# Kernel optimization log

Hardware: AMD Instinct MI355X
Metric: run time of the kernel (lower is better)

Reference implementation:

```python
import jax, jax.numpy as jnp
import numpy as np
import math

NUM_HEADS = 16
LOGIT_SCALE_MAX = math.log(1.0 / 0.01)  # log(100)
EPS = 1e-12


def _l2norm(x):
    # F.normalize(x, dim=-1): x / max(||x||_2, eps)
    n = jnp.sqrt(jnp.sum(x * x, axis=-1, keepdims=True))
    return x / jnp.maximum(n, EPS)


def setup_inputs() -> dict:
    key = jax.random.key(0)
    ks = jax.random.split(key, 6)
    N, B, C = 1024, 4, 1024
    scale = (C // NUM_HEADS) ** -0.5
    return {
        "query": jax.random.normal(ks[0], (N, B, C), jnp.float32),
        "key": jax.random.normal(ks[1], (N, B, C), jnp.float32),
        "value": jax.random.normal(ks[2], (N, B, C), jnp.float32),
        "in_proj_w": jax.random.normal(ks[3], (3 * C, C), jnp.float32) * scale,
        "in_proj_b": jnp.zeros((3 * C,), jnp.float32),
        "logit_scale": jnp.log(10.0) * jnp.ones((NUM_HEADS, 1, 1), jnp.float32),
        "out_w": jax.random.normal(ks[4], (C, C), jnp.float32) * scale,
        "out_b": jnp.zeros((C,), jnp.float32),
    }


def reference(query, key, value, in_proj_w, in_proj_b, logit_scale, out_w, out_b):
    N, B, C = query.shape
    H = NUM_HEADS
    hd = C // H
    # packed in-projection, split into q/k/v pieces
    w_q, w_k, w_v = jnp.split(in_proj_w, 3, axis=0)
    b_q, b_k, b_v = jnp.split(in_proj_b, 3, axis=0)
    q = query @ w_q.T + b_q          # (N, B, C)
    k = key @ w_k.T + b_k
    v = value @ w_v.T + b_v
    # (N, B, C) -> (B*H, N, hd)
    q = q.reshape(N, B * H, hd).swapaxes(0, 1)
    k = k.reshape(N, B * H, hd).swapaxes(0, 1)
    v = v.reshape(N, B * H, hd).swapaxes(0, 1)
    # cosine-similarity scores with learnable per-head logit scale
    attn = jnp.einsum('bqd,bkd->bqk', _l2norm(q), _l2norm(k))  # (B*H, N, N)
    ls = jnp.exp(jnp.minimum(logit_scale, LOGIT_SCALE_MAX))     # (H,1,1)
    attn = (attn.reshape(B, H, N, N) * ls).reshape(B * H, N, N)
    attn = jax.nn.softmax(attn, axis=-1)
    x = jnp.einsum('bqk,bkd->bqd', attn, v)                     # (B*H, N, hd)
    x = x.swapaxes(0, 1).reshape(N, B, C)
    return x @ out_w.T + out_b
```

## Files before the change

kernel.cpp:

```cpp
#include <hip/hip_runtime.h>


typedef _Float16 f16x8 __attribute__((ext_vector_type(8)));
typedef float    f32x4 __attribute__((ext_vector_type(4)));

#define LOG2E 1.4426950408889634f
#define LOGMAX 4.6051702f

#define GLOAD16(g, l) \
    __builtin_amdgcn_global_load_lds((__attribute__((address_space(1))) void*)(g), \
                                     (__attribute__((address_space(3))) void*)(l), 16, 0, 0)

__device__ __forceinline__ unsigned short f2h(float x) {
    union { _Float16 h; unsigned short u; } cv;
    cv.h = (_Float16)x;
    return cv.u;
}

__global__ __launch_bounds__(256) void cvt_all(
    const float* __restrict__ q, const float* __restrict__ k,
    const float* __restrict__ v, const float* __restrict__ w,
    const float* __restrict__ ow,
    unsigned short* __restrict__ qbf, unsigned short* __restrict__ kbf,
    unsigned short* __restrict__ vbf, unsigned short* __restrict__ wbf,
    unsigned short* __restrict__ owbf)
{
    int b = blockIdx.x;
    const float* src; unsigned short* dst; int idx;
    if      (b < 4096)  { src = q;  dst = qbf;  idx = b; }
    else if (b < 8192)  { src = k;  dst = kbf;  idx = b - 4096; }
    else if (b < 12288) { src = v;  dst = vbf;  idx = b - 8192; }
    else if (b < 15360) { src = w;  dst = wbf;  idx = b - 12288; }
    else                { src = ow; dst = owbf; idx = b - 15360; }
    int i = idx * 256 + threadIdx.x;
    float4 val = ((const float4*)src)[i];
    ushort4 o;
    o.x = f2h(val.x); o.y = f2h(val.y); o.z = f2h(val.z); o.w = f2h(val.w);
    ((ushort4*)dst)[i] = o;
}

__global__ __launch_bounds__(256) void proj_gemm(
    const unsigned short* __restrict__ qbf, const unsigned short* __restrict__ kbf,
    const unsigned short* __restrict__ vbf, const unsigned short* __restrict__ wbf,
    const float* __restrict__ bias, const float* __restrict__ lsc,
    unsigned short* __restrict__ qn, unsigned short* __restrict__ kn,
    unsigned short* __restrict__ vT)
{
    __shared__ __align__(16) unsigned short AsmF[128 * 64];
    __shared__ __align__(16) unsigned short BsmF[128 * 64];
    int tid = threadIdx.x;
    int lane = tid & 63, wave = tid >> 6;
    int lr = lane & 15, lq = lane >> 4;
    int wr = wave >> 1, wc = wave & 1;

    int lin = blockIdx.x;
    int xcd = lin & 7, s = lin >> 3;
    int xt = s & 7, yy = (s >> 3) & 3, z = s >> 5;
    int m0 = (xcd * 4 + yy) * 128, n0 = xt * 128;

    const unsigned short* A = (z == 0) ? qbf : (z == 1) ? kbf : vbf;
    const unsigned short* W = wbf + (size_t)z * 1024 * 1024;

    int rl = lane >> 3;
    int cg = ((lane & 7) ^ rl) << 3;
    const unsigned short* gA = A + (size_t)(m0 + wave * 32 + rl) * 1024 + cg;
    const unsigned short* gB = W + (size_t)(n0 + wave * 32 + rl) * 1024 + cg;
    unsigned short* lA = &AsmF[wave * 32 * 64];
    unsigned short* lB = &BsmF[wave * 32 * 64];

    int swz = lr & 7;
    int c0 = (lq ^ swz) << 3;
    int c1 = ((lq ^ 4) ^ swz) << 3;

    f32x4 acc[4][4];
    for (int i = 0; i < 4; i++) for (int j = 0; j < 4; j++) acc[i][j] = (f32x4){0.f, 0.f, 0.f, 0.f};

    for (int ki = 0; ki < 16; ++ki) {
        for (int j = 0; j < 4; ++j) {
            GLOAD16(gA + ki * 64 + j * 8192, lA + j * 512);
            GLOAD16(gB + ki * 64 + j * 8192, lB + j * 512);
        }
        __syncthreads();
        for (int kc = 0; kc < 2; ++kc) {
            int co = kc ? c1 : c0;
            f16x8 af[4], bfr[4];
            for (int mi = 0; mi < 4; ++mi) af[mi]  = *(const f16x8*)&AsmF[(wr * 64 + mi * 16 + lr) * 64 + co];
            for (int ni = 0; ni < 4; ++ni) bfr[ni] = *(const f16x8*)&BsmF[(wc * 64 + ni * 16 + lr) * 64 + co];
            for (int mi = 0; mi < 4; ++mi)
                for (int ni = 0; ni < 4; ++ni)
                    acc[mi][ni] = __builtin_amdgcn_mfma_f32_16x16x32_f16(af[mi], bfr[ni], acc[mi][ni], 0, 0, 0);
        }
        __syncthreads();
    }

    int h = (n0 >> 6) + wc;
    float bv[4];
    for (int ni = 0; ni < 4; ++ni) bv[ni] = bias[z * 1024 + n0 + wc * 64 + ni * 16 + lr];
    for (int mi = 0; mi < 4; ++mi)
        for (int ni = 0; ni < 4; ++ni)
            for (int r = 0; r < 4; ++r) acc[mi][ni][r] += bv[ni];

    float lsfac = __expf(fminf(lsc[h], LOGMAX)) * LOG2E;

    for (int mi = 0; mi < 4; ++mi)
        for (int r = 0; r < 4; ++r) {
            int row = m0 + wr * 64 + mi * 16 + lq * 4 + r;
            int n = row >> 2, b = row & 3;
            int bh = b * 16 + h;
            if (z < 2) {
                float ss = 0.f;
                for (int ni = 0; ni < 4; ++ni) ss += acc[mi][ni][r] * acc[mi][ni][r];
                for (int off = 1; off < 16; off <<= 1) ss += __shfl_xor(ss, off);
                float scale = 1.0f / fmaxf(sqrtf(ss), 1e-12f);
                if (z == 0) scale *= lsfac;
                unsigned short* dst = (z == 0) ? qn : kn;
                for (int ni = 0; ni < 4; ++ni)
                    dst[(size_t)bh * 65536 + (size_t)n * 64 + ni * 16 + lr] = f2h(acc[mi][ni][r] * scale);
            } else {
                for (int ni = 0; ni < 4; ++ni)
                    vT[(size_t)bh * 65536 + (size_t)(ni * 16 + lr) * 1024 + n] = f2h(acc[mi][ni][r]);
            }
        }
}

__global__ __launch_bounds__(256) void flash_kernel(
    const unsigned short* __restrict__ qn, const unsigned short* __restrict__ kn,
    const unsigned short* __restrict__ vT, const float* __restrict__ lsc,
    unsigned short* __restrict__ xb)
{
    __shared__ __align__(16) unsigned short K_flat[64 * 64];
    __shared__ __align__(16) unsigned short V_flat[64 * 64];
    __shared__ __align__(16) unsigned short P_lds[4][2][16][72];
    int tid = threadIdx.x;
    int lane = tid & 63, wave = tid >> 6;
    int lr = lane & 15, lq = lane >> 4;

    int lin = blockIdx.x;
    int xcd = lin & 7, s = lin >> 3;
    int qt = s & 7, bh = xcd * 8 + (s >> 3);
    int q0 = qt * 128;

    float off = __expf(fminf(lsc[bh & 15], LOGMAX)) * LOG2E - 12.0f;
    f32x4 initv = (f32x4){-off, -off, -off, -off};

    f16x8 qf[2][2];
    for (int g = 0; g < 2; ++g)
        for (int kc = 0; kc < 2; ++kc)
            qf[g][kc] = *(const f16x8*)(qn + (size_t)bh * 65536 +
                          (size_t)(q0 + g * 64 + wave * 16 + lr) * 64 + kc * 32 + lq * 8);

    int rl = lane >> 3;
    int cg = ((lane & 7) ^ rl) << 3;
    const unsigned short* gK = kn + (size_t)bh * 65536 + (size_t)(wave * 16 + rl) * 64 + cg;
    const unsigned short* gV = vT + (size_t)bh * 65536 + (size_t)(wave * 16 + rl) * 1024 + cg;
    unsigned short* lK = &K_flat[wave * 16 * 64];
    unsigned short* lV = &V_flat[wave * 16 * 64];
    int swz = lr & 7;
    int c0 = (lq ^ swz) << 3;
    int c1 = ((lq ^ 4) ^ swz) << 3;

    f32x4 o[2][4];
    for (int g = 0; g < 2; ++g) for (int i = 0; i < 4; i++) o[g][i] = (f32x4){0.f, 0.f, 0.f, 0.f};
    float lsum[2] = {0.f, 0.f};

    for (int kt = 0; kt < 16; ++kt) {
        for (int j = 0; j < 2; ++j) {
            GLOAD16(gK + kt * 4096 + j * 512,  lK + j * 512);
            GLOAD16(gV + kt * 64  + j * 8192,  lV + j * 512);
        }
        __syncthreads();

        f32x4 sc[2][4];
        for (int ct = 0; ct < 4; ++ct) {
            for (int kc = 0; kc < 2; ++kc) {
                f16x8 kf = *(const f16x8*)&K_flat[(ct * 16 + lr) * 64 + (kc ? c1 : c0)];
                for (int g = 0; g < 2; ++g)
                    sc[g][ct] = __builtin_amdgcn_mfma_f32_16x16x32_f16(
                        kf, qf[g][kc], kc == 0 ? initv : sc[g][ct], 0, 0, 0);
            }
        }

        for (int g = 0; g < 2; ++g)
            for (int ct = 0; ct < 4; ++ct) {
                float p0 = exp2f(sc[g][ct][0]), p1 = exp2f(sc[g][ct][1]);
                float p2 = exp2f(sc[g][ct][2]), p3 = exp2f(sc[g][ct][3]);
                lsum[g] += (p0 + p1) + (p2 + p3);
                ushort4 pw;
                pw.x = f2h(p0); pw.y = f2h(p1); pw.z = f2h(p2); pw.w = f2h(p3);
                *(ushort4*)&P_lds[wave][g][lr][ct * 16 + lq * 4] = pw;
            }

        f16x8 pf[2][2];
        for (int g = 0; g < 2; ++g)
            for (int kc = 0; kc < 2; ++kc)
                pf[g][kc] = *(const f16x8*)&P_lds[wave][g][lr][kc * 32 + lq * 8];
        for (int nt = 0; nt < 4; ++nt)
            for (int kc = 0; kc < 2; ++kc) {
                f16x8 vf = *(const f16x8*)&V_flat[(nt * 16 + lr) * 64 + (kc ? c1 : c0)];
                for (int g = 0; g < 2; ++g)
                    o[g][nt] = __builtin_amdgcn_mfma_f32_16x16x32_f16(vf, pf[g][kc], o[g][nt], 0, 0, 0);
            }
        __syncthreads();
    }

    int b = bh >> 4, h = bh & 15;
    for (int g = 0; g < 2; ++g) {
        float ls = lsum[g];
        ls += __shfl_xor(ls, 16);
        ls += __shfl_xor(ls, 32);
        float inv = 1.0f / ls;
        size_t m = (size_t)(q0 + g * 64 + wave * 16 + lr) * 4 + b;
        for (int nt = 0; nt < 4; ++nt) {
            ushort4 w;
            w.x = f2h(o[g][nt][0] * inv); w.y = f2h(o[g][nt][1] * inv);
            w.z = f2h(o[g][nt][2] * inv); w.w = f2h(o[g][nt][3] * inv);
            *(ushort4*)(xb + m * 1024 + h * 64 + nt * 16 + lq * 4) = w;
        }
    }
}

__global__ __launch_bounds__(256) void out_gemm(
    const unsigned short* __restrict__ xb, const unsigned short* __restrict__ owbf,
    const float* __restrict__ bias, float* __restrict__ outp)
{
    __shared__ __align__(16) unsigned short AsmF[128 * 64];
    __shared__ __align__(16) unsigned short BsmF[64 * 64];
    int tid = threadIdx.x;
    int lane = tid & 63, wave = tid >> 6;
    int lr = lane & 15, lq = lane >> 4;

    int lin = blockIdx.x;
    int xcd = lin & 7, s = lin >> 3;
    int xt = s & 15, yy = s >> 4;
    int m0 = (xcd * 4 + yy) * 128, n0 = xt * 64;

    int rl = lane >> 3;
    int cg = ((lane & 7) ^ rl) << 3;
    const unsigned short* gA = xb   + (size_t)(m0 + wave * 32 + rl) * 1024 + cg;
    const unsigned short* gB = owbf + (size_t)(n0 + wave * 16 + rl) * 1024 + cg;
    unsigned short* lA = &AsmF[wave * 32 * 64];
    unsigned short* lB = &BsmF[wave * 16 * 64];
    int swz = lr & 7;
    int c0 = (lq ^ swz) << 3;
    int c1 = ((lq ^ 4) ^ swz) << 3;

    f32x4 acc[2][4];
    for (int i = 0; i < 2; i++) for (int j = 0; j < 4; j++) acc[i][j] = (f32x4){0.f, 0.f, 0.f, 0.f};

    for (int ki = 0; ki < 16; ++ki) {
        for (int j = 0; j < 4; ++j)
            GLOAD16(gA + ki * 64 + j * 8192, lA + j * 512);
        for (int j = 0; j < 2; ++j)
            GLOAD16(gB + ki * 64 + j * 8192, lB + j * 512);
        __syncthreads();
        for (int kc = 0; kc < 2; ++kc) {
            int co = kc ? c1 : c0;
            f16x8 af[2], bfr[4];
            for (int mi = 0; mi < 2; ++mi) af[mi]  = *(const f16x8*)&AsmF[(wave * 32 + mi * 16 + lr) * 64 + co];
            for (int ni = 0; ni < 4; ++ni) bfr[ni] = *(const f16x8*)&BsmF[(ni * 16 + lr) * 64 + co];
            for (int mi = 0; mi < 2; ++mi)
                for (int ni = 0; ni < 4; ++ni)
                    acc[mi][ni] = __builtin_amdgcn_mfma_f32_16x16x32_f16(af[mi], bfr[ni], acc[mi][ni], 0, 0, 0);
        }
        __syncthreads();
    }
    for (int mi = 0; mi < 2; ++mi)
        for (int ni = 0; ni < 4; ++ni)
            for (int r = 0; r < 4; ++r) {
                int row = m0 + wave * 32 + mi * 16 + lq * 4 + r;
                int col = n0 + ni * 16 + lr;
                outp[(size_t)row * 1024 + col] = acc[mi][ni][r] + bias[col];
            }
}

extern "C" void kernel_launch(void* const* d_in, const int* in_sizes, int n_in,
                              void* d_out, int out_size, void* d_ws, size_t ws_size,
                              hipStream_t stream) {
    const float* query = (const float*)d_in[0];
    const float* key   = (const float*)d_in[1];
    const float* value = (const float*)d_in[2];
    const float* ipw   = (const float*)d_in[3];
    const float* ipb   = (const float*)d_in[4];
    const float* lsc   = (const float*)d_in[5];
    const float* ow    = (const float*)d_in[6];
    const float* ob    = (const float*)d_in[7];
    float* outp = (float*)d_out;

    char* ws = (char*)d_ws;
    unsigned short* qbf  = (unsigned short*)(ws);
    unsigned short* kbf  = (unsigned short*)(ws + 8388608);
    unsigned short* vbf  = (unsigned short*)(ws + 16777216);
    unsigned short* wbf  = (unsigned short*)(ws + 25165824);
    unsigned short* owbf = (unsigned short*)(ws + 31457280);
    unsigned short* qn   = (unsigned short*)(ws + 33554432);
    unsigned short* kn   = (unsigned short*)(ws + 41943040);
    unsigned short* vT   = (unsigned short*)(ws + 50331648);
    unsigned short* xbuf = (unsigned short*)(ws + 58720256);

    cvt_all<<<16384, 256, 0, stream>>>(query, key, value, ipw, ow,
                                       qbf, kbf, vbf, wbf, owbf);
    proj_gemm<<<768, 256, 0, stream>>>(qbf, kbf, vbf, wbf, ipb, lsc, qn, kn, vT);
    flash_kernel<<<512, 256, 0, stream>>>(qn, kn, vT, lsc, xbuf);
    out_gemm<<<512, 256, 0, stream>>>(xbuf, owbf, ob, outp);
}
```

Baseline: 207.0 us.

## Double-buffer K/V tiles in flash kernel and use packed fp16 conversion

Splits the K and V LDS tiles into two buffers so the next tile's global-to-LDS loads are issued while the current tile is computed, with one barrier per iteration instead of two. It also switches to the raw exp2 builtin and packed round-toward-zero fp16 conversion for the probabilities, and raises wave priority around the MFMA blocks. The intent is to hide load latency and cut VALU work in the softmax step. The cost is twice the LDS for K/V, which may lower occupancy, plus RTZ rounding instead of round-to-nearest.

```diff
diff --git a/kernel.cpp b/kernel.cpp
--- a/kernel.cpp
+++ b/kernel.cpp
@@ -2,6 +2,7 @@
 
 
 typedef _Float16 f16x8 __attribute__((ext_vector_type(8)));
+typedef __fp16   h16x2 __attribute__((ext_vector_type(2)));
 typedef float    f32x4 __attribute__((ext_vector_type(4)));
 
 #define LOG2E 1.4426950408889634f
@@ -128,8 +129,8 @@
     const unsigned short* __restrict__ vT, const float* __restrict__ lsc,
     unsigned short* __restrict__ xb)
 {
-    __shared__ __align__(16) unsigned short K_flat[64 * 64];
-    __shared__ __align__(16) unsigned short V_flat[64 * 64];
+    __shared__ __align__(16) unsigned short K_flat[2][64 * 64];
+    __shared__ __align__(16) unsigned short V_flat[2][64 * 64];
     __shared__ __align__(16) unsigned short P_lds[4][2][16][72];
     int tid = threadIdx.x;
     int lane = tid & 63, wave = tid >> 6;
@@ -153,8 +154,6 @@
     int cg = ((lane & 7) ^ rl) << 3;
     const unsigned short* gK = kn + (size_t)bh * 65536 + (size_t)(wave * 16 + rl) * 64 + cg;
     const unsigned short* gV = vT + (size_t)bh * 65536 + (size_t)(wave * 16 + rl) * 1024 + cg;
-    unsigned short* lK = &K_flat[wave * 16 * 64];
-    unsigned short* lV = &V_flat[wave * 16 * 64];
     int swz = lr & 7;
     int c0 = (lq ^ swz) << 3;
     int c1 = ((lq ^ 4) ^ swz) << 3;
@@ -163,44 +162,65 @@
     for (int g = 0; g < 2; ++g) for (int i = 0; i < 4; i++) o[g][i] = (f32x4){0.f, 0.f, 0.f, 0.f};
     float lsum[2] = {0.f, 0.f};
 
+    {
+        unsigned short* lK = &K_flat[0][wave * 16 * 64];
+        unsigned short* lV = &V_flat[0][wave * 16 * 64];
+        for (int j = 0; j < 2; ++j) {
+            GLOAD16(gK + j * 512,  lK + j * 512);
+            GLOAD16(gV + j * 8192, lV + j * 512);
+        }
+    }
+
     for (int kt = 0; kt < 16; ++kt) {
-        for (int j = 0; j < 2; ++j) {
-            GLOAD16(gK + kt * 4096 + j * 512,  lK + j * 512);
-            GLOAD16(gV + kt * 64  + j * 8192,  lV + j * 512);
-        }
-        __syncthreads();
+        int cur = kt & 1;
+        __syncthreads();
+
+        if (kt < 15) {
+            unsigned short* lK = &K_flat[cur ^ 1][wave * 16 * 64];
+            unsigned short* lV = &V_flat[cur ^ 1][wave * 16 * 64];
+            for (int j = 0; j < 2; ++j) {
+                GLOAD16(gK + (kt + 1) * 4096 + j * 512,  lK + j * 512);
+                GLOAD16(gV + (kt + 1) * 64  + j * 8192,  lV + j * 512);
+            }
+        }
 
         f32x4 sc[2][4];
+        __builtin_amdgcn_s_setprio(1);
         for (int ct = 0; ct < 4; ++ct) {
             for (int kc = 0; kc < 2; ++kc) {
-                f16x8 kf = *(const f16x8*)&K_flat[(ct * 16 + lr) * 64 + (kc ? c1 : c0)];
+                f16x8 kf = *(const f16x8*)&K_flat[cur][(ct * 16 + lr) * 64 + (kc ? c1 : c0)];
                 for (int g = 0; g < 2; ++g)
                     sc[g][ct] = __builtin_amdgcn_mfma_f32_16x16x32_f16(
                         kf, qf[g][kc], kc == 0 ? initv : sc[g][ct], 0, 0, 0);
             }
         }
+        __builtin_amdgcn_s_setprio(0);
 
         for (int g = 0; g < 2; ++g)
             for (int ct = 0; ct < 4; ++ct) {
-                float p0 = exp2f(sc[g][ct][0]), p1 = exp2f(sc[g][ct][1]);
-                float p2 = exp2f(sc[g][ct][2]), p3 = exp2f(sc[g][ct][3]);
+                float p0 = __builtin_amdgcn_exp2f(sc[g][ct][0]);
+                float p1 = __builtin_amdgcn_exp2f(sc[g][ct][1]);
+                float p2 = __builtin_amdgcn_exp2f(sc[g][ct][2]);
+                float p3 = __builtin_amdgcn_exp2f(sc[g][ct][3]);
                 lsum[g] += (p0 + p1) + (p2 + p3);
-                ushort4 pw;
-                pw.x = f2h(p0); pw.y = f2h(p1); pw.z = f2h(p2); pw.w = f2h(p3);
-                *(ushort4*)&P_lds[wave][g][lr][ct * 16 + lq * 4] = pw;
+                union { h16x2 h[2]; ushort4 u; } pw;
+                pw.h[0] = __builtin_amdgcn_cvt_pkrtz(p0, p1);
+                pw.h[1] = __builtin_amdgcn_cvt_pkrtz(p2, p3);
+                *(ushort4*)&P_lds[wave][g][lr][ct * 16 + lq * 4] = pw.u;
             }
 
         f16x8 pf[2][2];
         for (int g = 0; g < 2; ++g)
             for (int kc = 0; kc < 2; ++kc)
                 pf[g][kc] = *(const f16x8*)&P_lds[wave][g][lr][kc * 32 + lq * 8];
+        __builtin_amdgcn_s_setprio(1);
         for (int nt = 0; nt < 4; ++nt)
             for (int kc = 0; kc < 2; ++kc) {
-                f16x8 vf = *(const f16x8*)&V_flat[(nt * 16 + lr) * 64 + (kc ? c1 : c0)];
+                f16x8 vf = *(const f16x8*)&V_flat[cur][(nt * 16 + lr) * 64 + (kc ? c1 : c0)];
                 for (int g = 0; g < 2; ++g)
                     o[g][nt] = __builtin_amdgcn_mfma_f32_16x16x32_f16(vf, pf[g][kc], o[g][nt], 0, 0, 0);
             }
-        __syncthreads();
+        __builtin_amdgcn_s_setprio(0);
     }
 
     int b = bh >> 4, h = bh & 15;
```

Result: no change. 203.8 us (-1.6%).

## Halve flash query tile to 64 rows, doubling grid; add setprio and fast exp/cvt

Applied to the files above, without the earlier changes.

Each flash block now handles 64 query rows instead of 128, so the grid doubles to 1024 blocks and register and LDS use per block drop, which should raise occupancy. The MFMA phases are wrapped in s_setprio to favour matrix issue. The softmax path now uses the hardware exp2 builtin and packed round-toward-zero f16 conversion. The cost is twice as much K/V tile loading from global memory for the same work, and slightly different rounding of P.

```diff
diff --git a/kernel.cpp b/kernel.cpp
--- a/kernel.cpp
+++ b/kernel.cpp
@@ -2,6 +2,7 @@
 
 
 typedef _Float16 f16x8 __attribute__((ext_vector_type(8)));
+typedef __fp16   h16x2 __attribute__((ext_vector_type(2)));
 typedef float    f32x4 __attribute__((ext_vector_type(4)));
 
 #define LOG2E 1.4426950408889634f
@@ -130,24 +131,23 @@
 {
     __shared__ __align__(16) unsigned short K_flat[64 * 64];
     __shared__ __align__(16) unsigned short V_flat[64 * 64];
-    __shared__ __align__(16) unsigned short P_lds[4][2][16][72];
+    __shared__ __align__(16) unsigned short P_lds[4][16][72];
     int tid = threadIdx.x;
     int lane = tid & 63, wave = tid >> 6;
     int lr = lane & 15, lq = lane >> 4;
 
     int lin = blockIdx.x;
     int xcd = lin & 7, s = lin >> 3;
-    int qt = s & 7, bh = xcd * 8 + (s >> 3);
-    int q0 = qt * 128;
+    int qt = s & 15, bh = xcd * 8 + (s >> 4);
+    int q0 = qt * 64;
 
     float off = __expf(fminf(lsc[bh & 15], LOGMAX)) * LOG2E - 12.0f;
     f32x4 initv = (f32x4){-off, -off, -off, -off};
 
-    f16x8 qf[2][2];
-    for (int g = 0; g < 2; ++g)
-        for (int kc = 0; kc < 2; ++kc)
-            qf[g][kc] = *(const f16x8*)(qn + (size_t)bh * 65536 +
-                          (size_t)(q0 + g * 64 + wave * 16 + lr) * 64 + kc * 32 + lq * 8);
+    f16x8 qf[2];
+    for (int kc = 0; kc < 2; ++kc)
+        qf[kc] = *(const f16x8*)(qn + (size_t)bh * 65536 +
+                      (size_t)(q0 + wave * 16 + lr) * 64 + kc * 32 + lq * 8);
 
     int rl = lane >> 3;
     int cg = ((lane & 7) ^ rl) << 3;
@@ -159,9 +159,9 @@
     int c0 = (lq ^ swz) << 3;
     int c1 = ((lq ^ 4) ^ swz) << 3;
 
-    f32x4 o[2][4];
-    for (int g = 0; g < 2; ++g) for (int i = 0; i < 4; i++) o[g][i] = (f32x4){0.f, 0.f, 0.f, 0.f};
-    float lsum[2] = {0.f, 0.f};
+    f32x4 o[4];
+    for (int i = 0; i < 4; i++) o[i] = (f32x4){0.f, 0.f, 0.f, 0.f};
+    float lsum = 0.f;
 
     for (int kt = 0; kt < 16; ++kt) {
         for (int j = 0; j < 2; ++j) {
@@ -170,52 +170,52 @@
         }
         __syncthreads();
 
-        f32x4 sc[2][4];
-        for (int ct = 0; ct < 4; ++ct) {
+        f32x4 sc[4];
+        __builtin_amdgcn_s_setprio(1);
+        for (int ct = 0; ct < 4; ++ct)
             for (int kc = 0; kc < 2; ++kc) {
                 f16x8 kf = *(const f16x8*)&K_flat[(ct * 16 + lr) * 64 + (kc ? c1 : c0)];
-                for (int g = 0; g < 2; ++g)
-                    sc[g][ct] = __builtin_amdgcn_mfma_f32_16x16x32_f16(
-                        kf, qf[g][kc], kc == 0 ? initv : sc[g][ct], 0, 0, 0);
+                sc[ct] = __builtin_amdgcn_mfma_f32_16x16x32_f16(
+                    kf, qf[kc], kc == 0 ? initv : sc[ct], 0, 0, 0);
             }
-        }
-
-        for (int g = 0; g < 2; ++g)
-            for (int ct = 0; ct < 4; ++ct) {
-                float p0 = exp2f(sc[g][ct][0]), p1 = exp2f(sc[g][ct][1]);
-                float p2 = exp2f(sc[g][ct][2]), p3 = exp2f(sc[g][ct][3]);
-                lsum[g] += (p0 + p1) + (p2 + p3);
-                ushort4 pw;
-                pw.x = f2h(p0); pw.y = f2h(p1); pw.z = f2h(p2); pw.w = f2h(p3);
-                *(ushort4*)&P_lds[wave][g][lr][ct * 16 + lq * 4] = pw;
-            }
-
-        f16x8 pf[2][2];
-        for (int g = 0; g < 2; ++g)
-            for (int kc = 0; kc < 2; ++kc)
-                pf[g][kc] = *(const f16x8*)&P_lds[wave][g][lr][kc * 32 + lq * 8];
+        __builtin_amdgcn_s_setprio(0);
+
+        for (int ct = 0; ct < 4; ++ct) {
+            float p0 = __builtin_amdgcn_exp2f(sc[ct][0]);
+            float p1 = __builtin_amdgcn_exp2f(sc[ct][1]);
+            float p2 = __builtin_amdgcn_exp2f(sc[ct][2]);
+            float p3 = __builtin_amdgcn_exp2f(sc[ct][3]);
+            lsum += (p0 + p1) + (p2 + p3);
+            union { h16x2 h[2]; ushort4 u; } pw;
+            pw.h[0] = __builtin_amdgcn_cvt_pkrtz(p0, p1);
+            pw.h[1] = __builtin_amdgcn_cvt_pkrtz(p2, p3);
+            *(ushort4*)&P_lds[wave][lr][ct * 16 + lq * 4] = pw.u;
+        }
+
+        f16x8 pf[2];
+        for (int kc = 0; kc < 2; ++kc)
+            pf[kc] = *(const f16x8*)&P_lds[wave][lr][kc * 32 + lq * 8];
+        __builtin_amdgcn_s_setprio(1);
         for (int nt = 0; nt < 4; ++nt)
             for (int kc = 0; kc < 2; ++kc) {
                 f16x8 vf = *(const f16x8*)&V_flat[(nt * 16 + lr) * 64 + (kc ? c1 : c0)];
-                for (int g = 0; g < 2; ++g)
-                    o[g][nt] = __builtin_amdgcn_mfma_f32_16x16x32_f16(vf, pf[g][kc], o[g][nt], 0, 0, 0);
+                o[nt] = __builtin_amdgcn_mfma_f32_16x16x32_f16(vf, pf[kc], o[nt], 0, 0, 0);
             }
+        __builtin_amdgcn_s_setprio(0);
         __syncthreads();
     }
 
     int b = bh >> 4, h = bh & 15;
-    for (int g = 0; g < 2; ++g) {
-        float ls = lsum[g];
-        ls += __shfl_xor(ls, 16);
-        ls += __shfl_xor(ls, 32);
-        float inv = 1.0f / ls;
-        size_t m = (size_t)(q0 + g * 64 + wave * 16 + lr) * 4 + b;
-        for (int nt = 0; nt < 4; ++nt) {
-            ushort4 w;
-            w.x = f2h(o[g][nt][0] * inv); w.y = f2h(o[g][nt][1] * inv);
-            w.z = f2h(o[g][nt][2] * inv); w.w = f2h(o[g][nt][3] * inv);
-            *(ushort4*)(xb + m * 1024 + h * 64 + nt * 16 + lq * 4) = w;
-        }
+    float ls = lsum;
+    ls += __shfl_xor(ls, 16);
+    ls += __shfl_xor(ls, 32);
+    float inv = 1.0f / ls;
+    size_t m = (size_t)(q0 + wave * 16 + lr) * 4 + b;
+    for (int nt = 0; nt < 4; ++nt) {
+        ushort4 w;
+        w.x = f2h(o[nt][0] * inv); w.y = f2h(o[nt][1] * inv);
+        w.z = f2h(o[nt][2] * inv); w.w = f2h(o[nt][3] * inv);
+        *(ushort4*)(xb + m * 1024 + h * 64 + nt * 16 + lq * 4) = w;
     }
 }
 
@@ -300,6 +300,6 @@
     cvt_all<<<16384, 256, 0, stream>>>(query, key, value, ipw, ow,
                                        qbf, kbf, vbf, wbf, owbf);
     proj_gemm<<<768, 256, 0, stream>>>(qbf, kbf, vbf, wbf, ipb, lsc, qn, kn, vT);
-    flash_kernel<<<512, 256, 0, stream>>>(qn, kn, vT, lsc, xbuf);
+    flash_kernel<<<1024, 256, 0, stream>>>(qn, kn, vT, lsc, xbuf);
     out_gemm<<<512, 256, 0, stream>>>(xbuf, owbf, ob, outp);
 }
```

Result: faster. 202.0 us (-2.4%).
